# Performance work log

Hardware: AMD Instinct MI355X
Metric: run time of the kernel (lower is better)

Reference implementation:

```python
import jax, jax.numpy as jnp
import numpy as np

H, B, N, D, VD, FFH = 8, 16, 512, 512, 64, 2048
NPICK = N // 2
NORM = 1.0 / np.sqrt(VD)


def _ha_encoder(h, W_query, W_key, W_val, W1, W2, W3, W4, W5, W6):
    # h: [B, N, D]; weights: [H, D, VD]
    np_ = NPICK
    pick, dlv = h[:, :np_], h[:, np_:]
    proj = lambda x, W: jnp.einsum('bnd,hdk->hbnk', x, W)
    Q, K, V = proj(h, W_query), proj(h, W_key), proj(h, W_val)
    Kp, Kd = K[:, :, :np_], K[:, :, np_:]   # shared projections (same W_key)
    Vp, Vd = V[:, :, :np_], V[:, :, np_:]
    Qp = proj(pick, W1); Qpap = proj(pick, W2); Qpad = proj(pick, W3)
    Qd = proj(dlv, W4);  Qdad = proj(dlv, W5);  Qdap = proj(dlv, W6)
    c_main = NORM * jnp.einsum('hbnk,hbmk->hbnm', Q, K)          # [H,B,N,N]
    c_pd = NORM * jnp.sum(Qp * Kd, -1)                           # [H,B,np] paired pick->delivery
    c_pap = NORM * jnp.einsum('hbnk,hbmk->hbnm', Qpap, Kp)       # pick -> all pick
    c_pad = NORM * jnp.einsum('hbnk,hbmk->hbnm', Qpad, Kd)       # pick -> all delivery
    c_dp = NORM * jnp.sum(Qd * Kp, -1)                           # paired delivery->pick
    c_dad = NORM * jnp.einsum('hbnk,hbmk->hbnm', Qdad, Kd)       # delivery -> all delivery
    c_dap = NORM * jnp.einsum('hbnk,hbmk->hbnm', Qdap, Kp)       # delivery -> all pick
    ninf1 = jnp.full((H, h.shape[0], np_), -jnp.inf, c_main.dtype)
    ninf2 = jnp.full((H, h.shape[0], np_, np_), -jnp.inf, c_main.dtype)
    col_pd = jnp.concatenate([c_pd, ninf1], 2)[..., None]        # [H,B,N,1]
    blk_pap = jnp.concatenate([c_pap, ninf2], 2)                 # [H,B,N,np]
    blk_pad = jnp.concatenate([c_pad, ninf2], 2)
    col_dp = jnp.concatenate([ninf1, c_dp], 2)[..., None]
    blk_dad = jnp.concatenate([ninf2, c_dad], 2)
    blk_dap = jnp.concatenate([ninf2, c_dap], 2)
    compat = jnp.concatenate([c_main, col_pd, blk_pap, blk_pad, col_dp, blk_dad, blk_dap], -1)
    a = jax.nn.softmax(compat, -1)                               # [H,B,N,N+2+4*np]
    zpad = jnp.zeros_like(Vd)
    V_add_d = jnp.concatenate([Vd, zpad], 2)                     # [H,B,N,VD]
    V_add_p = jnp.concatenate([zpad, Vp], 2)
    av = lambda w, v: jnp.einsum('hbnm,hbmv->hbnv', w, v)
    i = N
    heads = av(a[..., :N], V)
    heads = heads + a[..., i:i + 1] * V_add_d; i += 1
    heads = heads + av(a[..., i:i + np_], Vp); i += np_
    heads = heads + av(a[..., i:i + np_], Vd); i += np_
    heads = heads + a[..., i:i + 1] * V_add_p; i += 1
    heads = heads + av(a[..., i:i + np_], Vd); i += np_
    heads = heads + av(a[..., i:i + np_], Vp)
    return heads.transpose(1, 2, 0, 3).reshape(h.shape[0], N, H * VD)


def _split_heads(x):
    b, n, hd = x.shape
    return x.reshape(b, n, H, hd // H).transpose(0, 2, 1, 3)


def _mha(q, k, v):
    dk = q.shape[-1]
    w = jax.nn.softmax(jnp.einsum('bhnd,bhmd->bhnm', q, k) / np.sqrt(dk), -1)
    o = jnp.einsum('bhnm,bhmd->bhnd', w, v)
    b, hh, n, d = o.shape
    return o.transpose(0, 2, 1, 3).reshape(b, n, hh * d)


def _ff(x, w1, b1, w2, b2, a):
    return x + (jax.nn.relu(x @ w1 + b1) @ w2 + b2) * a


def _forward(x, W_query, W_key, W_val, W1_query, W2_query, W3_query, W4_query, W5_query, W6_query,
             Wq_w, Wk_w, Wv_w, Wq2p_w, Wq2d_w, Wk2_w, Wv2_w,
             comb_w, comb_b, comb2_w, comb2_b, comb3_w, comb3_b,
             alpha1, alpha2, alpha3,
             ff1_w1, ff1_b1, ff1_w2, ff1_b2, ffa1,
             ff2_w1, ff2_b1, ff2_w2, ff2_b2, ffa2,
             ff3_w1, ff3_b1, ff3_w2, ff3_b2, ffa3):
    # stage 1: heterogeneous attention block (combine_3 / AN3 / FF3)
    ha = _ha_encoder(x, W_query, W_key, W_val, W1_query, W2_query, W3_query, W4_query, W5_query, W6_query)
    out = x + (ha @ comb3_w + comb3_b) * alpha3
    out = _ff(out, ff3_w1, ff3_b1, ff3_w2, ff3_b2, ffa3)
    # stage 2: standard multi-head self-attention (combine / AN1 / FF1)
    q = _split_heads(out @ Wq_w); k = _split_heads(out @ Wk_w); v = _split_heads(out @ Wv_w)
    out = out + (_mha(q, k, v) @ comb_w + comb_b) * alpha1
    out = _ff(out, ff1_w1, ff1_b1, ff1_w2, ff1_b2, ffa1)
    # stage 3: pickup/delivery specific queries (combine_2 / AN2 / FF2)
    q2 = jnp.concatenate([out[:, :NPICK] @ Wq2p_w, out[:, NPICK:] @ Wq2d_w], 1)
    q2 = _split_heads(q2); k2 = _split_heads(out @ Wk2_w); v2 = _split_heads(out @ Wv2_w)
    out = out + (_mha(q2, k2, v2) @ comb2_w + comb2_b) * alpha2
    out = _ff(out, ff2_w1, ff2_b1, ff2_w2, ff2_b2, ffa2)
    return out


def setup_inputs() -> dict:
    key = jax.random.key(0)
    ks = jax.random.split(key, 64)
    it = iter(range(64))
    def nrm(shape):
        return jax.random.normal(ks[next(it)], shape, jnp.float32)
    def uni(shape):
        s = 1.0 / np.sqrt(shape[-1])  # torch init_parameters: uniform(-1/sqrt(size(-1)), ...)
        return jax.random.uniform(ks[next(it)], shape, jnp.float32, -s, s)
    d = {'x': nrm((B, N, D))}
    for n in ['W_query', 'W_key', 'W_val', 'W1_query', 'W2_query', 'W3_query', 'W4_query', 'W5_query', 'W6_query']:
        d[n] = uni((H, D, VD))
    for n in ['Wq_w', 'Wk_w', 'Wv_w', 'Wq2p_w', 'Wq2d_w', 'Wk2_w', 'Wv2_w']:
        d[n] = uni((D, H * VD))
    for n in ['comb_w', 'comb2_w', 'comb3_w']:
        d[n] = uni((H * VD, D))
    for n in ['comb_b', 'comb2_b', 'comb3_b']:
        d[n] = uni((D,))
    for n in ['alpha1', 'alpha2', 'alpha3']:
        d[n] = uni((1,))
    for i in ['1', '2', '3']:
        d['ff' + i + '_w1'] = uni((D, FFH))
        d['ff' + i + '_b1'] = uni((FFH,))
        d['ff' + i + '_w2'] = uni((FFH, D))
        d['ff' + i + '_b2'] = uni((D,))
        d['ffa' + i] = uni((1,))
    return d


def reference(x, W_query, W_key, W_val, W1_query, W2_query, W3_query, W4_query, W5_query, W6_query,
              Wq_w, Wk_w, Wv_w, Wq2p_w, Wq2d_w, Wk2_w, Wv2_w,
              comb_w, comb_b, comb2_w, comb2_b, comb3_w, comb3_b,
              alpha1, alpha2, alpha3,
              ff1_w1, ff1_b1, ff1_w2, ff1_b2, ffa1,
              ff2_w1, ff2_b1, ff2_w2, ff2_b2, ffa2,
              ff3_w1, ff3_b1, ff3_w2, ff3_b2, ffa3):
    return _forward(x, W_query, W_key, W_val, W1_query, W2_query, W3_query, W4_query, W5_query, W6_query,
                    Wq_w, Wk_w, Wv_w, Wq2p_w, Wq2d_w, Wk2_w, Wv2_w,
                    comb_w, comb_b, comb2_w, comb2_b, comb3_w, comb3_b,
                    alpha1, alpha2, alpha3,
                    ff1_w1, ff1_b1, ff1_w2, ff1_b2, ffa1,
                    ff2_w1, ff2_b1, ff2_w2, ff2_b2, ffa2,
                    ff3_w1, ff3_b1, ff3_w2, ff3_b2, ffa3)
```

## Files before the change

kernel.cpp:

```cpp
#include <hip/hip_runtime.h>
#include <math.h>

#define Hh 8
#define Bb 16
#define Nn 512
#define Dd 512
#define VDd 64
#define NPICKk 256
#define NORMF 0.125f
#define SCL2 0.1803368801f

typedef unsigned short ushortT;
typedef __bf16 bf16x8 __attribute__((ext_vector_type(8)));
typedef float f32x4 __attribute__((ext_vector_type(4)));

struct PtrsB { const ushortT* p[12]; };
struct PtrsD { ushortT* p[6]; };
struct Ptrs9 { const float* p[9]; };
struct Ptrs10 { const float* p[10]; };
struct Ptrs6 { const float* p[6]; };

__device__ inline ushortT f2bf(float f) {
    __bf16 h = (__bf16)f;
    union { __bf16 h; ushortT u; } v; v.h = h;
    return v.u;
}
__device__ inline float bf2f(ushortT u) {
    union { unsigned int u; float f; } v; v.u = ((unsigned int)u) << 16;
    return v.f;
}
__device__ inline float exp2fast(float x) {
#if __has_builtin(__builtin_amdgcn_exp2f)
    return __builtin_amdgcn_exp2f(x);
#else
    return exp2f(x);
#endif
}
__device__ inline void gload16(const void* gptr, void* ldsptr) {
    auto g = reinterpret_cast<const __attribute__((address_space(1))) unsigned int*>(
        reinterpret_cast<uintptr_t>(gptr));
    auto l = reinterpret_cast<__attribute__((address_space(3))) unsigned int*>(
        reinterpret_cast<uintptr_t>(ldsptr));
    __builtin_amdgcn_global_load_lds(g, l, 16, 0, 0);
}

#define LIX(r, g) (((r) << 6) + ((((g) ^ ((r) & 7))) << 3))

__global__ __launch_bounds__(256) void castx(const float* __restrict__ in,
                                             ushortT* __restrict__ out) {
    int i = blockIdx.x * 256 + threadIdx.x;
    float4 v = *(const float4*)&in[(size_t)i * 4];
    ushort4 o; o.x = f2bf(v.x); o.y = f2bf(v.y); o.z = f2bf(v.z); o.w = f2bf(v.w);
    *(ushort4*)&out[(size_t)i * 4] = o;
}

__device__ inline void tbody(const float* __restrict__ in, ushortT* __restrict__ out,
                             int in_ld, int out_ld, int r0, int c0) {
    __shared__ float T[64][65];
    int tr = threadIdx.x >> 4, tc4 = (threadIdx.x & 15) * 4;
#pragma unroll
    for (int p = 0; p < 4; ++p) {
        float4 v = *(const float4*)&in[(size_t)(r0 + tr + p * 16) * in_ld + c0 + tc4];
        T[tr + p * 16][tc4 + 0] = v.x; T[tr + p * 16][tc4 + 1] = v.y;
        T[tr + p * 16][tc4 + 2] = v.z; T[tr + p * 16][tc4 + 3] = v.w;
    }
    __syncthreads();
#pragma unroll
    for (int p = 0; p < 4; ++p) {
        int orow = c0 + tr + p * 16;
        int ocol = r0 + tc4;
        ushort4 o;
        o.x = f2bf(T[tc4 + 0][tr + p * 16]);
        o.y = f2bf(T[tc4 + 1][tr + p * 16]);
        o.z = f2bf(T[tc4 + 2][tr + p * 16]);
        o.w = f2bf(T[tc4 + 3][tr + p * 16]);
        *(ushort4*)&out[(size_t)orow * out_ld + ocol] = o;
    }
}

__global__ __launch_bounds__(256) void thead(Ptrs9 s, ushortT* __restrict__ dst) {
    int w = blockIdx.z >> 3, h = blockIdx.z & 7;
    tbody(s.p[w] + (size_t)h * 512 * 64,
          dst + (size_t)w * 262144 + (size_t)h * 64 * 512,
          64, 512, blockIdx.y * 64, 0);
}
__global__ __launch_bounds__(256) void tsq(Ptrs10 s, ushortT* __restrict__ dst) {
    tbody(s.p[blockIdx.z], dst + (size_t)blockIdx.z * 262144,
          512, 512, blockIdx.y * 64, blockIdx.x * 64);
}
__global__ __launch_bounds__(256) void tff(Ptrs6 s, ushortT* __restrict__ dst) {
    int z = blockIdx.z;
    if (z < 3) { if (blockIdx.y >= 8 || blockIdx.x >= 32) return; }
    else       { if (blockIdx.y >= 32 || blockIdx.x >= 8) return; }
    int in_ld = (z < 3) ? 2048 : 512;
    int out_ld = (z < 3) ? 512 : 2048;
    tbody(s.p[z], dst + (size_t)z * 1048576, in_ld, out_ld,
          blockIdx.y * 64, blockIdx.x * 64);
}

__global__ __launch_bounds__(256) void gemm_bf(
    PtrsB Bp, PtrsD Db, const ushortT* __restrict__ A, float* __restrict__ outF,
    int M, int N, int K, const float* __restrict__ bias,
    const float* __restrict__ res, const float* __restrict__ alpha,
    int do_relu, int nroute, int vtmask, int scmask)
{
    __shared__ __align__(16) ushortT As[2][128 * 64];
    __shared__ __align__(16) ushortT Bs[2][128 * 64];
    const int tid = threadIdx.x;
    const int wid = tid >> 6, lane = tid & 63;
    const int wm = wid >> 1, wn = wid & 1;
    const int l15 = lane & 15, l4 = lane >> 4;

    int bid = blockIdx.y * gridDim.x + blockIdx.x;
    int nwg = gridDim.x * gridDim.y;
    int q = nwg >> 3;
    int swz = (bid & 7) * q + (bid >> 3);
    int bx = swz % gridDim.x, by = swz / gridDim.x;

    const int r0 = by * 128, c0 = bx * 128;
    const int half = ((r0 & (Nn - 1)) >= NPICKk) ? 1 : 0;
    const ushortT* Bt = Bp.p[((c0 >> 9) << 1) | half];
    const int cB = nroute ? (c0 & 511) : c0;

    const ushortT* aSrc[4];
    const ushortT* bSrc[4];
    int offv[4];
#pragma unroll
    for (int i = 0; i < 4; ++i) {
        int off = wid * 4096 + i * 1024 + lane * 16;
        int row = off >> 7;
        int sg = ((off >> 4) & 7) ^ (row & 7);
        aSrc[i] = A + (size_t)(r0 + row) * K + sg * 8;
        bSrc[i] = Bt + (size_t)(cB + row) * K + sg * 8;
        offv[i] = off;
    }

    const int nkt = K >> 6;
#pragma unroll
    for (int i = 0; i < 4; ++i) {
        gload16(aSrc[i], (char*)As[0] + offv[i]);
        gload16(bSrc[i], (char*)Bs[0] + offv[i]);
    }
#pragma unroll
    for (int i = 0; i < 4; ++i) {
        gload16(aSrc[i] + 64, (char*)As[1] + offv[i]);
        gload16(bSrc[i] + 64, (char*)Bs[1] + offv[i]);
    }

    f32x4 acc[4][4] = {};

    for (int t = 0; t < nkt; ++t) {
        const int cur = t & 1;
        if (t == nkt - 1) asm volatile("s_waitcnt vmcnt(0)" ::: "memory");
        else              asm volatile("s_waitcnt vmcnt(8)" ::: "memory");
        __builtin_amdgcn_s_barrier();
        __builtin_amdgcn_sched_barrier(0);
        const ushortT* Ac = As[cur];
        const ushortT* Bc = Bs[cur];
#pragma unroll
        for (int kk = 0; kk < 2; ++kk) {
            int g0 = kk * 4 + l4;
            bf16x8 af[4], bfv[4];
#pragma unroll
            for (int mi = 0; mi < 4; ++mi)
                af[mi] = *(const bf16x8*)&Ac[LIX(wm * 64 + mi * 16 + l15, g0)];
#pragma unroll
            for (int ni = 0; ni < 4; ++ni)
                bfv[ni] = *(const bf16x8*)&Bc[LIX(wn * 64 + ni * 16 + l15, g0)];
#pragma unroll
            for (int mi = 0; mi < 4; ++mi)
#pragma unroll
                for (int ni = 0; ni < 4; ++ni)
                    acc[mi][ni] = __builtin_amdgcn_mfma_f32_16x16x32_bf16(
                        bfv[ni], af[mi], acc[mi][ni], 0, 0, 0);
        }
        __builtin_amdgcn_s_barrier();
        asm volatile("" ::: "memory");
        if (t + 2 < nkt) {
            int kt2 = (t + 2) << 6;
#pragma unroll
            for (int i = 0; i < 4; ++i) {
                gload16(aSrc[i] + kt2, (char*)As[cur] + offv[i]);
                gload16(bSrc[i] + kt2, (char*)Bs[cur] + offv[i]);
            }
        }
    }

    if (nroute) {
#pragma unroll
        for (int mi = 0; mi < 4; ++mi) {
            int row = r0 + wm * 64 + mi * 16 + l15;
#pragma unroll
            for (int ni = 0; ni < 4; ++ni) {
                int col = c0 + wn * 64 + ni * 16 + l4 * 4;
                int range = col >> 9, cc = col & 511;
                ushortT* d = Db.p[range];
                f32x4 a = acc[mi][ni];
                if ((scmask >> range) & 1) {
                    a[0] *= SCL2; a[1] *= SCL2; a[2] *= SCL2; a[3] *= SCL2;
                }
                if ((vtmask >> range) & 1) {
                    size_t vb = ((size_t)(row >> 9) * Hh + (cc >> 6)) * 64 + (cc & 63);
                    int tok = row & 511;
#pragma unroll
                    for (int r = 0; r < 4; ++r)
                        d[((vb + r) << 9) + tok] = f2bf(a[r]);
                } else {
                    ushort4 o;
                    o.x = f2bf(a[0]); o.y = f2bf(a[1]);
                    o.z = f2bf(a[2]); o.w = f2bf(a[3]);
                    *(ushort4*)&d[((size_t)row << 9) + cc] = o;
                }
            }
        }
    } else {
        const float alp = alpha ? alpha[0] : 1.0f;
        ushortT* outB = Db.p[0];
#pragma unroll
        for (int mi = 0; mi < 4; ++mi) {
            int row = r0 + wm * 64 + mi * 16 + l15;
#pragma unroll
            for (int ni = 0; ni < 4; ++ni) {
                int colb = c0 + wn * 64 + ni * 16 + l4 * 4;
                f32x4 a = acc[mi][ni];
                if (bias) {
                    float4 b4 = *(const float4*)&bias[colb];
                    a[0] += b4.x; a[1] += b4.y; a[2] += b4.z; a[3] += b4.w;
                }
                if (do_relu) {
#pragma unroll
                    for (int r = 0; r < 4; ++r) a[r] = fmaxf(a[r], 0.f);
                }
#pragma unroll
                for (int r = 0; r < 4; ++r) a[r] *= alp;
                size_t idx = (size_t)row * N + colb;
                if (res) {
                    float4 r4 = *(const float4*)&res[idx];
                    a[0] += r4.x; a[1] += r4.y; a[2] += r4.z; a[3] += r4.w;
                }
                if (outF)
                    *(float4*)&outF[idx] = make_float4(a[0], a[1], a[2], a[3]);
                if (outB) {
                    ushort4 o;
                    o.x = f2bf(a[0]); o.y = f2bf(a[1]);
                    o.z = f2bf(a[2]); o.w = f2bf(a[3]);
                    *(ushort4*)&outB[idx] = o;
                }
            }
        }
    }
}

__global__ __launch_bounds__(256) void gemm64(
    const ushortT* __restrict__ Bw, const ushortT* __restrict__ A,
    float* __restrict__ outF, ushortT* __restrict__ outB,
    int M, int N, int K, const float* __restrict__ bias,
    const float* __restrict__ resf, const ushortT* __restrict__ resb,
    const float* __restrict__ alpha, int do_relu)
{
    __shared__ __align__(16) ushortT As[64 * 64];
    __shared__ __align__(16) ushortT Bs[128 * 64];
    const int tid = threadIdx.x;
    const int wid = tid >> 6, lane = tid & 63;
    const int wm = wid >> 1, wn = wid & 1;
    const int l15 = lane & 15, l4 = lane >> 4;

    int bid = blockIdx.y * gridDim.x + blockIdx.x;
    int nwg = gridDim.x * gridDim.y;
    int q = nwg >> 3;
    int swz = (bid & 7) * q + (bid >> 3);
    int bx = swz % gridDim.x, by = swz / gridDim.x;
    const int r0 = by * 64, c0 = bx * 128;

    const ushortT* aSrc[2];
    char* ldsA[2];
#pragma unroll
    for (int i = 0; i < 2; ++i) {
        int off = wid * 2048 + i * 1024 + lane * 16;
        int row = off >> 7;
        int sg = ((off >> 4) & 7) ^ (row & 7);
        aSrc[i] = A + (size_t)(r0 + row) * K + sg * 8;
        ldsA[i] = (char*)As + off;
    }
    const ushortT* bSrc[4];
    char* ldsB[4];
#pragma unroll
    for (int i = 0; i < 4; ++i) {
        int off = wid * 4096 + i * 1024 + lane * 16;
        int row = off >> 7;
        int sg = ((off >> 4) & 7) ^ (row & 7);
        bSrc[i] = Bw + (size_t)(c0 + row) * K + sg * 8;
        ldsB[i] = (char*)Bs + off;
    }

    f32x4 acc[2][4] = {};

    for (int kt = 0; kt < K; kt += 64) {
        __syncthreads();
#pragma unroll
        for (int i = 0; i < 2; ++i) gload16(aSrc[i] + kt, ldsA[i]);
#pragma unroll
        for (int i = 0; i < 4; ++i) gload16(bSrc[i] + kt, ldsB[i]);
        asm volatile("s_waitcnt vmcnt(0)" ::: "memory");
        __syncthreads();
#pragma unroll
        for (int kk = 0; kk < 2; ++kk) {
            int g0 = kk * 4 + l4;
            bf16x8 af[2], bfv[4];
#pragma unroll
            for (int mi = 0; mi < 2; ++mi)
                af[mi] = *(const bf16x8*)&As[LIX(wm * 32 + mi * 16 + l15, g0)];
#pragma unroll
            for (int ni = 0; ni < 4; ++ni)
                bfv[ni] = *(const bf16x8*)&Bs[LIX(wn * 64 + ni * 16 + l15, g0)];
#pragma unroll
            for (int mi = 0; mi < 2; ++mi)
#pragma unroll
                for (int ni = 0; ni < 4; ++ni)
                    acc[mi][ni] = __builtin_amdgcn_mfma_f32_16x16x32_bf16(
                        bfv[ni], af[mi], acc[mi][ni], 0, 0, 0);
        }
    }

    const float alp = alpha ? alpha[0] : 1.0f;
#pragma unroll
    for (int mi = 0; mi < 2; ++mi) {
        int row = r0 + wm * 32 + mi * 16 + l15;
#pragma unroll
        for (int ni = 0; ni < 4; ++ni) {
            int colb = c0 + wn * 64 + ni * 16 + l4 * 4;
            f32x4 a = acc[mi][ni];
            if (bias) {
                float4 b4 = *(const float4*)&bias[colb];
                a[0] += b4.x; a[1] += b4.y; a[2] += b4.z; a[3] += b4.w;
            }
            if (do_relu) {
#pragma unroll
                for (int r = 0; r < 4; ++r) a[r] = fmaxf(a[r], 0.f);
            }
#pragma unroll
            for (int r = 0; r < 4; ++r) a[r] *= alp;
            size_t idx = (size_t)row * N + colb;
            if (resf) {
                float4 r4 = *(const float4*)&resf[idx];
                a[0] += r4.x; a[1] += r4.y; a[2] += r4.z; a[3] += r4.w;
            }
            if (resb) {
                ushort4 r4 = *(const ushort4*)&resb[idx];
                a[0] += bf2f(r4.x); a[1] += bf2f(r4.y);
                a[2] += bf2f(r4.z); a[3] += bf2f(r4.w);
            }
            if (outF)
                *(float4*)&outF[idx] = make_float4(a[0], a[1], a[2], a[3]);
            if (outB) {
                ushort4 o;
                o.x = f2bf(a[0]); o.y = f2bf(a[1]);
                o.z = f2bf(a[2]); o.w = f2bf(a[3]);
                *(ushort4*)&outB[idx] = o;
            }
        }
    }
}

__global__ __launch_bounds__(256) void diag_dot_bb(const ushortT* __restrict__ QD,
                                                   const ushortT* __restrict__ K,
                                                   float* __restrict__ Sdg) {
    int i = blockIdx.x * 256 + threadIdx.x;
    int h = i & 7, n = (i >> 3) & 511, b = i >> 12;
    int dix = (n < NPICKk) ? n + NPICKk : n - NPICKk;
    const ushortT* q = QD + (((size_t)(b * Nn + n) * Hh + h) << 6);
    const ushortT* k = K + (((size_t)(b * Nn + dix) * Hh + h) << 6);
    float s = 0.f;
#pragma unroll
    for (int d = 0; d < 64; d += 4) {
        ushort4 a = *(const ushort4*)(q + d);
        ushort4 c = *(const ushort4*)(k + d);
        s += bf2f(a.x) * bf2f(c.x) + bf2f(a.y) * bf2f(c.y)
           + bf2f(a.z) * bf2f(c.z) + bf2f(a.w) * bf2f(c.w);
    }
    Sdg[i] = s;
}

template <int HA>
__global__ __launch_bounds__(256) void attn10(
    const ushortT* __restrict__ Qm, const ushortT* __restrict__ Km,
    const ushortT* __restrict__ Vtm, const ushortT* __restrict__ QAm,
    const ushortT* __restrict__ QBm, const float* __restrict__ Sdg,
    ushortT* __restrict__ Out)
{
    __shared__ __align__(16) ushortT Ks[64 * 64];
    __shared__ __align__(16) ushortT Vs[64 * 64];
    __shared__ __align__(16) ushortT Pw[4][16 * 64];
    __shared__ float sdl[64];

    const int tid = threadIdx.x, wid = tid >> 6, lane = tid & 63;
    const int l15 = lane & 15, l4 = lane >> 4;

    const int p = blockIdx.x + (blockIdx.y << 3) + (blockIdx.z << 6);
    const int n0 = (((p >> 3) & 7)) << 6;
    const int g8 = (p & 7) | ((p >> 6) << 3);
    const int h = g8 & 7, b = g8 >> 3;
    const int bh = b * Hh + h;

    const size_t qrow = (((size_t)(b * Nn + n0 + wid * 16 + l15) * Hh + h) << 6);
    bf16x8 qf[2], xaf[2], xbf[2];
#pragma unroll
    for (int kk = 0; kk < 2; ++kk) {
        int g0 = kk * 4 + l4;
        qf[kk] = *(const bf16x8*)&Qm[qrow + g0 * 8];
        if (HA) {
            xaf[kk] = *(const bf16x8*)&QAm[qrow + g0 * 8];
            xbf[kk] = *(const bf16x8*)&QBm[qrow + g0 * 8];
        }
    }
    if (HA && tid < 64) sdl[tid] = Sdg[((size_t)(b * Nn + n0 + tid)) * Hh + h];
    const int td = (n0 < NPICKk) ? ((n0 + NPICKk) >> 6) : ((n0 - NPICKk) >> 6);

    const ushortT* kSrc[2]; ushortT* kDst[2];
    const ushortT* vSrc[2]; ushortT* vDst[2];
#pragma unroll
    for (int i = 0; i < 2; ++i) {
        int off = wid * 2048 + i * 1024 + lane * 16;
        int row = off >> 7, sg = ((off >> 4) & 7) ^ (row & 7);
        kSrc[i] = Km + (((size_t)(b * Nn + row) * Hh + h) << 6) + sg * 8;
        kDst[i] = (ushortT*)((char*)Ks + off);
        vSrc[i] = Vtm + (((size_t)(bh * 64 + row)) << 9) + sg * 8;
        vDst[i] = (ushortT*)((char*)Vs + off);
    }

    float M[4], Lp[4];
    f32x4 Oa[4] = {};
#pragma unroll
    for (int r = 0; r < 4; ++r) { M[r] = -INFINITY; Lp[r] = 0.f; }

    bf16x8 krbuf[2][2], vrbuf[2][2];
#pragma unroll
    for (int i = 0; i < 2; ++i) {
        krbuf[0][i] = *(const bf16x8*)kSrc[i];
        vrbuf[0][i] = *(const bf16x8*)vSrc[i];
    }

#pragma unroll
    for (int t = 0; t < 8; ++t) {
        const int cur = t & 1, nxt = cur ^ 1;
        __builtin_amdgcn_s_barrier();
#pragma unroll
        for (int i = 0; i < 2; ++i) {
            *(bf16x8*)kDst[i] = krbuf[cur][i];
            *(bf16x8*)vDst[i] = vrbuf[cur][i];
        }
        if (t < 7) {
#pragma unroll
            for (int i = 0; i < 2; ++i) {
                krbuf[nxt][i] = *(const bf16x8*)(kSrc[i] + (size_t)(t + 1) * (64 * Hh * VDd));
                vrbuf[nxt][i] = *(const bf16x8*)(vSrc[i] + (t + 1) * 64);
            }
        }
        asm volatile("s_waitcnt lgkmcnt(0)" ::: "memory");
        __builtin_amdgcn_s_barrier();
        __builtin_amdgcn_sched_barrier(0);

        __builtin_amdgcn_s_setprio(1);
        f32x4 s1[4] = {}, sX[4] = {};
#pragma unroll
        for (int kk = 0; kk < 2; ++kk) {
            bf16x8 aq = qf[kk];
            bf16x8 ax;
            if (HA) ax = (t >= 4) ? xbf[kk] : xaf[kk];
#pragma unroll
            for (int ni = 0; ni < 4; ++ni) {
                bf16x8 bk = *(const bf16x8*)&Ks[LIX(ni * 16 + l15, kk * 4 + l4)];
                s1[ni] = __builtin_amdgcn_mfma_f32_16x16x32_bf16(aq, bk, s1[ni], 0, 0, 0);
                if (HA)
                    sX[ni] = __builtin_amdgcn_mfma_f32_16x16x32_bf16(ax, bk, sX[ni], 0, 0, 0);
            }
        }
        __builtin_amdgcn_s_setprio(0);

        const bool dt = HA && (t == td);

        float mloc[4];
        bool grow = false;
#pragma unroll
        for (int r = 0; r < 4; ++r) {
            int rw = wid * 16 + l4 * 4 + r;
            float m = s1[0][r];
#pragma unroll
            for (int ni = 1; ni < 4; ++ni) m = fmaxf(m, s1[ni][r]);
            if (HA) {
#pragma unroll
                for (int ni = 0; ni < 4; ++ni) m = fmaxf(m, sX[ni][r]);
            }
            if (dt && l15 == l4 * 4 + r) m = fmaxf(m, sdl[rw]);
            mloc[r] = m;
            grow = grow || (m > M[r] + 8.f);
        }
        if (__any(grow)) {
#pragma unroll
            for (int r = 0; r < 4; ++r) {
                float m = mloc[r];
#pragma unroll
                for (int o = 8; o >= 1; o >>= 1) m = fmaxf(m, __shfl_xor(m, o, 16));
                float mn = fmaxf(M[r], m);
                float sc = exp2fast(M[r] - mn);
                M[r] = mn; Lp[r] *= sc;
#pragma unroll
                for (int ni = 0; ni < 4; ++ni) Oa[ni][r] *= sc;
            }
        }

#pragma unroll
        for (int r = 0; r < 4; ++r) {
            int rw = wid * 16 + l4 * 4 + r;
            float rs = 0.f;
#pragma unroll
            for (int ni = 0; ni < 4; ++ni) {
                float pv = exp2fast(s1[ni][r] - M[r]);
                if (HA) pv += exp2fast(sX[ni][r] - M[r]);
                if (dt && ni == wid && l15 == l4 * 4 + r) pv += exp2fast(sdl[rw] - M[r]);
                s1[ni][r] = pv;
                rs += pv;
            }
            Lp[r] += rs;
        }

#pragma unroll
        for (int ni = 0; ni < 4; ++ni)
#pragma unroll
            for (int r = 0; r < 4; ++r) {
                int prow = l4 * 4 + r;
                int col = ni * 16 + l15;
                Pw[wid][(prow << 6) + ((((col >> 3) ^ (prow & 7))) << 3) + (col & 7)] =
                    f2bf(s1[ni][r]);
            }

        __builtin_amdgcn_s_setprio(1);
#pragma unroll
        for (int kk = 0; kk < 2; ++kk) {
            int g0 = kk * 4 + l4;
            bf16x8 ap = *(const bf16x8*)&Pw[wid][LIX(l15, g0)];
#pragma unroll
            for (int ni = 0; ni < 4; ++ni) {
                bf16x8 bv = *(const bf16x8*)&Vs[LIX(ni * 16 + l15, g0)];
                Oa[ni] = __builtin_amdgcn_mfma_f32_16x16x32_bf16(ap, bv, Oa[ni], 0, 0, 0);
            }
        }
        __builtin_amdgcn_s_setprio(0);
    }

#pragma unroll
    for (int r = 0; r < 4; ++r) {
        float l = Lp[r];
#pragma unroll
        for (int o = 8; o >= 1; o >>= 1) l += __shfl_xor(l, o, 16);
        float inv = 1.0f / l;
        size_t obase = (((size_t)(b * Nn + n0 + wid * 16 + l4 * 4 + r) * Hh + h) << 6);
#pragma unroll
        for (int ni = 0; ni < 4; ++ni)
            Out[obase + ni * 16 + l15] = f2bf(Oa[ni][r] * inv);
    }
}

extern "C" void kernel_launch(void* const* d_in, const int* in_sizes, int n_in,
                              void* d_out, int out_size, void* d_ws, size_t ws_size,
                              hipStream_t stream)
{
    const float* x = (const float*)d_in[0];

    int dictOrder = (in_sizes[18] != 512);
    const float* comb_w  = (const float*)d_in[17];
    const float* comb2_w = (const float*)d_in[dictOrder ? 18 : 19];
    const float* comb3_w = (const float*)d_in[dictOrder ? 19 : 21];
    const float* comb_b  = (const float*)d_in[dictOrder ? 20 : 18];
    const float* comb2_b = (const float*)d_in[dictOrder ? 21 : 20];
    const float* comb3_b = (const float*)d_in[22];
    const float* alpha1 = (const float*)d_in[23];
    const float* alpha2 = (const float*)d_in[24];
    const float* alpha3 = (const float*)d_in[25];
    const float* ff1_w1 = (const float*)d_in[26];
    const float* ff1_b1 = (const float*)d_in[27];
    const float* ff1_w2 = (const float*)d_in[28];
    const float* ff1_b2 = (const float*)d_in[29];
    const float* ffa1   = (const float*)d_in[30];
    const float* ff2_w1 = (const float*)d_in[31];
    const float* ff2_b1 = (const float*)d_in[32];
    const float* ff2_w2 = (const float*)d_in[33];
    const float* ff2_b2 = (const float*)d_in[34];
    const float* ffa2   = (const float*)d_in[35];
    const float* ff3_w1 = (const float*)d_in[36];
    const float* ff3_b1 = (const float*)d_in[37];
    const float* ff3_w2 = (const float*)d_in[38];
    const float* ff3_b2 = (const float*)d_in[39];
    const float* ffa3   = (const float*)d_in[40];

    char* W = (char*)d_ws;
    ushortT* wbHead = (ushortT*)(W + 0);
    ushortT* wbMha  = (ushortT*)(W + 4718592);
    ushortT* wbComb = (ushortT*)(W + 8388608);
    ushortT* wbFf1  = (ushortT*)(W + 9961472);
    ushortT* wbFf2  = (ushortT*)(W + 16252928);
    ushortT* xbf    = (ushortT*)(W + 22544384);
    float*   Sd     = (float*)  (W + 30932992);
    ushortT* bufQ   = (ushortT*)(W + 31195136);
    ushortT* bufK   = (ushortT*)(W + 39583744);
    ushortT* bufVt  = (ushortT*)(W + 47972352);
    ushortT* bufQA  = (ushortT*)(W + 56360960);
    ushortT* bufQB  = (ushortT*)(W + 64749568);
    ushortT* bufQD  = (ushortT*)(W + 73138176);
    ushortT* hidden = (ushortT*)(W + 81526784);
    ushortT* curb   = (ushortT*)(W + 115081216);
    ushortT* bufHA  = xbf;
    float*   cur    = (float*)d_out;

    dim3 tb(256);
    const int TOK = Bb * Nn;
    const size_t WS = 512 * 512;
    const size_t WF = 2048 * 512;

    hipLaunchKernelGGL(castx, dim3(TOK * 512 / 1024), tb, 0, stream, x, xbf);
    {
        Ptrs9 s; for (int i = 0; i < 9; ++i) s.p[i] = (const float*)d_in[1 + i];
        hipLaunchKernelGGL(thead, dim3(1, 8, 72), tb, 0, stream, s, wbHead);
    }
    {
        Ptrs10 s;
        for (int i = 0; i < 7; ++i) s.p[i] = (const float*)d_in[10 + i];
        s.p[7] = comb_w; s.p[8] = comb2_w; s.p[9] = comb3_w;
        hipLaunchKernelGGL(tsq, dim3(8, 8, 10), tb, 0, stream, s, wbMha);
    }
    {
        Ptrs6 s;
        s.p[0] = ff1_w1; s.p[1] = ff2_w1; s.p[2] = ff3_w1;
        s.p[3] = ff1_w2; s.p[4] = ff2_w2; s.p[5] = ff3_w2;
        hipLaunchKernelGGL(tff, dim3(32, 32, 6), tb, 0, stream, s, wbFf1);
    }

    auto gemm = [&](PtrsB Bp, PtrsD Db, const ushortT* A, float* oF,
                    int M, int Ncc, int Kc, const float* bias, const float* res,
                    const float* alp, int relu, int nroute, int vtmask, int scmask) {
        hipLaunchKernelGGL(gemm_bf, dim3(Ncc / 128, M / 128), tb, 0, stream,
                           Bp, Db, A, oF, M, Ncc, Kc, bias, res, alp, relu, nroute,
                           vtmask, scmask);
    };
    auto g64 = [&](const ushortT* Bw, const ushortT* A, float* oF, ushortT* oB,
                   int M, int Ncc, int Kc, const float* bias, const float* resf,
                   const ushortT* resb, const float* alp, int relu) {
        hipLaunchKernelGGL(gemm64, dim3(Ncc / 128, M / 64), tb, 0, stream,
                           Bw, A, oF, oB, M, Ncc, Kc, bias, resf, resb, alp, relu);
    };
    auto uni = [&](const ushortT* w) { PtrsB b; for (int i = 0; i < 12; ++i) b.p[i] = w; return b; };
    auto d1 = [&](ushortT* d) { PtrsD dd = {}; dd.p[0] = d; return dd; };

    {
        PtrsB b;
        b.p[0] = b.p[1] = wbHead + 0 * WS;
        b.p[2] = b.p[3] = wbHead + 1 * WS;
        b.p[4] = b.p[5] = wbHead + 2 * WS;
        b.p[6] = wbHead + 4 * WS; b.p[7] = wbHead + 8 * WS;
        b.p[8] = wbHead + 5 * WS; b.p[9] = wbHead + 7 * WS;
        b.p[10] = wbHead + 3 * WS; b.p[11] = wbHead + 6 * WS;
        PtrsD d; d.p[0] = bufQ; d.p[1] = bufK; d.p[2] = bufVt;
        d.p[3] = bufQA; d.p[4] = bufQB; d.p[5] = bufQD;
        gemm(b, d, xbf, nullptr, TOK, 3072, 512, nullptr, nullptr, nullptr, 0, 6, 4, 57);
    }

    hipLaunchKernelGGL(diag_dot_bb, dim3(Bb * Nn * Hh / 256), tb, 0, stream, bufQD, bufK, Sd);
    hipLaunchKernelGGL((attn10<1>), dim3(Nn / 64, Hh, Bb), tb, 0, stream,
                       bufQ, bufK, bufVt, bufQA, bufQB, Sd, bufHA);

    g64(wbComb + 2 * WS, bufHA, nullptr, curb, TOK, 512, 512, comb3_b, x, nullptr, alpha3, 0);
    gemm(uni(wbFf1 + 2 * WF), d1(hidden), curb, nullptr, TOK, 2048, 512, ff3_b1, nullptr, nullptr, 1, 0, 0, 0);
    g64(wbFf2 + 2 * WF, hidden, nullptr, curb, TOK, 512, 2048, ff3_b2, nullptr, curb, ffa3, 0);

    {
        PtrsB b;
        b.p[0] = b.p[1] = wbMha + 0 * WS;
        b.p[2] = b.p[3] = wbMha + 1 * WS;
        b.p[4] = b.p[5] = wbMha + 2 * WS;
        PtrsD d = {}; d.p[0] = bufQ; d.p[1] = bufK; d.p[2] = bufVt;
        gemm(b, d, curb, nullptr, TOK, 1536, 512, nullptr, nullptr, nullptr, 0, 3, 4, 1);
    }
    hipLaunchKernelGGL((attn10<0>), dim3(Nn / 64, Hh, Bb), tb, 0, stream,
                       bufQ, bufK, bufVt, nullptr, nullptr, nullptr, bufHA);
    g64(wbComb + 0 * WS, bufHA, nullptr, curb, TOK, 512, 512, comb_b, nullptr, curb, alpha1, 0);
    gemm(uni(wbFf1 + 0 * WF), d1(hidden), curb, nullptr, TOK, 2048, 512, ff1_b1, nullptr, nullptr, 1, 0, 0, 0);
    g64(wbFf2 + 0 * WF, hidden, nullptr, curb, TOK, 512, 2048, ff1_b2, nullptr, curb, ffa1, 0);

    {
        PtrsB b;
        b.p[0] = wbMha + 3 * WS; b.p[1] = wbMha + 4 * WS;
        b.p[2] = b.p[3] = wbMha + 5 * WS;
        b.p[4] = b.p[5] = wbMha + 6 * WS;
        PtrsD d = {}; d.p[0] = bufQ; d.p[1] = bufK; d.p[2] = bufVt;
        gemm(b, d, curb, nullptr, TOK, 1536, 512, nullptr, nullptr, nullptr, 0, 3, 4, 1);
    }
    hipLaunchKernelGGL((attn10<0>), dim3(Nn / 64, Hh, Bb), tb, 0, stream,
                       bufQ, bufK, bufVt, nullptr, nullptr, nullptr, bufHA);
    g64(wbComb + 1 * WS, bufHA, nullptr, curb, TOK, 512, 512, comb2_b, nullptr, curb, alpha2, 0);
    gemm(uni(wbFf1 + 1 * WF), d1(hidden), curb, nullptr, TOK, 2048, 512, ff2_b1, nullptr, nullptr, 1, 0, 0, 0);
    g64(wbFf2 + 1 * WF, hidden, cur, nullptr, TOK, 512, 2048, ff2_b2, nullptr, curb, ffa2, 0);
}
```

Before: 460.6 us.

## Double-buffer gemm64 LDS with prefetch-two pipeline and raise MFMA wave priority

```diff
diff --git a/kernel.cpp b/kernel.cpp
--- a/kernel.cpp
+++ b/kernel.cpp
@@ -157,6 +157,7 @@
         __builtin_amdgcn_sched_barrier(0);
         const ushortT* Ac = As[cur];
         const ushortT* Bc = Bs[cur];
+        __builtin_amdgcn_s_setprio(1);
 #pragma unroll
         for (int kk = 0; kk < 2; ++kk) {
             int g0 = kk * 4 + l4;
@@ -174,6 +175,7 @@
                     acc[mi][ni] = __builtin_amdgcn_mfma_f32_16x16x32_bf16(
                         bfv[ni], af[mi], acc[mi][ni], 0, 0, 0);
         }
+        __builtin_amdgcn_s_setprio(0);
         __builtin_amdgcn_s_barrier();
         asm volatile("" ::: "memory");
         if (t + 2 < nkt) {
@@ -258,8 +260,8 @@
     const float* __restrict__ resf, const ushortT* __restrict__ resb,
     const float* __restrict__ alpha, int do_relu)
 {
-    __shared__ __align__(16) ushortT As[64 * 64];
-    __shared__ __align__(16) ushortT Bs[128 * 64];
+    __shared__ __align__(16) ushortT As[2][64 * 64];
+    __shared__ __align__(16) ushortT Bs[2][128 * 64];
     const int tid = threadIdx.x;
     const int wid = tid >> 6, lane = tid & 63;
     const int wm = wid >> 1, wn = wid & 1;
@@ -273,52 +275,73 @@
     const int r0 = by * 64, c0 = bx * 128;
 
     const ushortT* aSrc[2];
-    char* ldsA[2];
+    int offA[2];
 #pragma unroll
     for (int i = 0; i < 2; ++i) {
         int off = wid * 2048 + i * 1024 + lane * 16;
         int row = off >> 7;
         int sg = ((off >> 4) & 7) ^ (row & 7);
         aSrc[i] = A + (size_t)(r0 + row) * K + sg * 8;
-        ldsA[i] = (char*)As + off;
+        offA[i] = off;
     }
     const ushortT* bSrc[4];
-    char* ldsB[4];
+    int offB[4];
 #pragma unroll
     for (int i = 0; i < 4; ++i) {
         int off = wid * 4096 + i * 1024 + lane * 16;
         int row = off >> 7;
         int sg = ((off >> 4) & 7) ^ (row & 7);
         bSrc[i] = Bw + (size_t)(c0 + row) * K + sg * 8;
-        ldsB[i] = (char*)Bs + off;
-    }
+        offB[i] = off;
+    }
+
+    const int nkt = K >> 6;
+#pragma unroll
+    for (int i = 0; i < 2; ++i) gload16(aSrc[i], (char*)As[0] + offA[i]);
+#pragma unroll
+    for (int i = 0; i < 4; ++i) gload16(bSrc[i], (char*)Bs[0] + offB[i]);
+#pragma unroll
+    for (int i = 0; i < 2; ++i) gload16(aSrc[i] + 64, (char*)As[1] + offA[i]);
+#pragma unroll
+    for (int i = 0; i < 4; ++i) gload16(bSrc[i] + 64, (char*)Bs[1] + offB[i]);
 
     f32x4 acc[2][4] = {};
 
-    for (int kt = 0; kt < K; kt += 64) {
-        __syncthreads();
-#pragma unroll
-        for (int i = 0; i < 2; ++i) gload16(aSrc[i] + kt, ldsA[i]);
-#pragma unroll
-        for (int i = 0; i < 4; ++i) gload16(bSrc[i] + kt, ldsB[i]);
-        asm volatile("s_waitcnt vmcnt(0)" ::: "memory");
-        __syncthreads();
+    for (int t = 0; t < nkt; ++t) {
+        const int cur = t & 1;
+        if (t == nkt - 1) asm volatile("s_waitcnt vmcnt(0)" ::: "memory");
+        else              asm volatile("s_waitcnt vmcnt(6)" ::: "memory");
+        __builtin_amdgcn_s_barrier();
+        __builtin_amdgcn_sched_barrier(0);
+        const ushortT* Ac = As[cur];
+        const ushortT* Bc = Bs[cur];
+        __builtin_amdgcn_s_setprio(1);
 #pragma unroll
         for (int kk = 0; kk < 2; ++kk) {
             int g0 = kk * 4 + l4;
             bf16x8 af[2], bfv[4];
 #pragma unroll
             for (int mi = 0; mi < 2; ++mi)
-                af[mi] = *(const bf16x8*)&As[LIX(wm * 32 + mi * 16 + l15, g0)];
+                af[mi] = *(const bf16x8*)&Ac[LIX(wm * 32 + mi * 16 + l15, g0)];
 #pragma unroll
             for (int ni = 0; ni < 4; ++ni)
-                bfv[ni] = *(const bf16x8*)&Bs[LIX(wn * 64 + ni * 16 + l15, g0)];
+                bfv[ni] = *(const bf16x8*)&Bc[LIX(wn * 64 + ni * 16 + l15, g0)];
 #pragma unroll
             for (int mi = 0; mi < 2; ++mi)
 #pragma unroll
                 for (int ni = 0; ni < 4; ++ni)
                     acc[mi][ni] = __builtin_amdgcn_mfma_f32_16x16x32_bf16(
                         bfv[ni], af[mi], acc[mi][ni], 0, 0, 0);
+        }
+        __builtin_amdgcn_s_setprio(0);
+        __builtin_amdgcn_s_barrier();
+        asm volatile("" ::: "memory");
+        if (t + 2 < nkt) {
+            int kt2 = (t + 2) << 6;
+#pragma unroll
+            for (int i = 0; i < 2; ++i) gload16(aSrc[i] + kt2, (char*)As[cur] + offA[i]);
+#pragma unroll
+            for (int i = 0; i < 4; ++i) gload16(bSrc[i] + kt2, (char*)Bs[cur] + offB[i]);
         }
     }
 
```

Measured after the change: 426.4 us, median of 3. -7.4%, faster.
